# Kernel optimization log

Measured on AMD Instinct MI355X. Metric: run time of the kernel, lower is better.

## Reference

```python
import jax, jax.numpy as jnp
import numpy as np

D = 256   # hidden_dim
N = 1024  # total nodes
NP = 384  # paratope nodes
NE = 384  # epitope nodes
NC = 14   # atom channels


def setup_inputs() -> dict:
    key = jax.random.key(0)
    ks = jax.random.split(key, 24)
    s = 1.0 / np.sqrt(D)
    s3 = 1.0 / np.sqrt(3 * D)
    w = lambda k, shape, sc: (jax.random.normal(k, shape, jnp.float32) * sc)
    z = lambda: jnp.zeros((D,), jnp.float32)
    return {
        "H": w(ks[0], (N, D), 1.0),
        "X": w(ks[1], (N, NC, 3), 1.0),
        "paratope_mask": jnp.zeros((N,), bool).at[:NP].set(True),
        "epitope_mask": jnp.zeros((N,), bool).at[NP:NP + NE].set(True),
        "res_w1": w(ks[2], (1, D), 1.0), "res_b1": z(),
        "res_w2": w(ks[3], (D, D), s), "res_b2": z(),
        "atom_w1": w(ks[4], (1, D), 1.0), "atom_b1": z(),
        "atom_w2": w(ks[5], (D, D), s), "atom_b2": z(),
        "sim_weight": jnp.float32(0.5),
        "int_w1": w(ks[6], (3 * D, D), s3), "int_b1": z(),
        "int_w2": w(ks[7], (D, D), s), "int_b2": z(),
        "wl": w(ks[8], (D, D), s),
        "wr": w(ks[9], (D, D), s),
        "wg_w": w(ks[10], (D, D), s), "wg_b": z(),
        "wq_w": w(ks[11], (D, D), s), "wq_b": z(),
        "wk_w": w(ks[12], (D, D), s), "wk_b": z(),
        "wv_w": w(ks[13], (D, D), s), "wv_b": z(),
    }


def _mlp2(x, w1, b1, w2, b2):
    return jax.nn.silu(x @ w1 + b1) @ w2 + b2


def reference(H, X, paratope_mask, epitope_mask,
              res_w1, res_b1, res_w2, res_b2,
              atom_w1, atom_b1, atom_w2, atom_b2,
              sim_weight,
              int_w1, int_b1, int_w2, int_b2,
              wl, wr, wg_w, wg_b, wq_w, wq_b, wk_w, wk_b, wv_w, wv_b):
    p_idx = jnp.nonzero(paratope_mask, size=NP)[0]
    e_idx = jnp.nonzero(epitope_mask, size=NE)[0]
    Hp = H[p_idx]                      # [NP, D]
    He = H[e_idx]                      # [NE, D]
    Xp_ca = X[p_idx, 1]                # [NP, 3] (CA atom)
    Xe_ca = X[e_idx, 1]                # [NE, 3]

    dX = Xp_ca[:, None, :] - Xe_ca[None, :, :]         # [NP, NE, 3]
    S = jnp.sum(dX * dX, axis=-1, keepdims=True)       # [NP, NE, 1]
    # original computes S_residue and S_atom with identical formula
    S_res = _mlp2(S, res_w1, res_b1, res_w2, res_b2)
    S_atom = _mlp2(S, atom_w1, atom_b1, atom_w2, atom_b2)
    wmix = jax.nn.sigmoid(sim_weight)
    S_comb = wmix * S_res + (1.0 - wmix) * S_atom      # [NP, NE, D]

    Hp_e = jnp.broadcast_to(Hp[:, None, :], (NP, NE, D))
    He_e = jnp.broadcast_to(He[None, :, :], (NP, NE, D))
    Z_in = jnp.concatenate([Hp_e, He_e, S_comb], axis=-1)  # [NP, NE, 3D]
    Z = _mlp2(Z_in, int_w1, int_b1, int_w2, int_b2)        # [NP, NE, D]

    I = (Hp @ wl)[:, None, :] * (He @ wr)[None, :, :]      # outer-product interaction
    gate = jax.nn.sigmoid(Z @ wg_w + wg_b)
    f_tri = gate * I

    Q = Z @ wq_w + wq_b
    K = Z @ wk_w + wk_b
    V = Z @ wv_w + wv_b
    scores = jnp.einsum('ped,pfd->pef', Q, K) / (D ** 0.5)  # [NP, NE, NE]
    A = jax.nn.softmax(scores, axis=-1)
    f_att = jnp.einsum('pef,pfd->ped', A, V)

    H_tri = f_tri + f_att                                   # [NP, NE, D]
    return H.at[p_idx].set(H_tri.mean(axis=1))
```

## Files before the change

### kernel.cpp

```cpp
#include <hip/hip_runtime.h>

#define NPAR 384
#define NEPI 384
#define DD   256
#define NTAB 4096
#define SMAX 96.0f
#define SDELTA (SMAX / NTAB)
#define SINVD (NTAB / SMAX)

using bf16x8 = __bf16 __attribute__((ext_vector_type(8)));
using bf16x2 = __bf16 __attribute__((ext_vector_type(2)));
using f32x4  = float __attribute__((ext_vector_type(4)));

#if defined(__has_builtin)
#if __has_builtin(__builtin_amdgcn_cvt_pk_bf16_f32)
#define HAVE_PK_BF16 1
#endif
#if __has_builtin(__builtin_amdgcn_rcpf)
#define HAVE_RCPF 1
#endif
#endif

__device__ __forceinline__ float fastrcp(float x) {
#ifdef HAVE_RCPF
  return __builtin_amdgcn_rcpf(x);
#else
  return 1.0f / x;
#endif
}
__device__ __forceinline__ float sigm(float x) { return fastrcp(1.0f + __expf(-x)); }
__device__ __forceinline__ float silu(float x) { return x * fastrcp(1.0f + __expf(-x)); }
__device__ __forceinline__ unsigned short f2bf(float f) {
  unsigned u = __float_as_uint(f);
  u += 0x7fffu + ((u >> 16) & 1u);
  return (unsigned short)(u >> 16);
}
__device__ __forceinline__ float bf2f(unsigned u16) {
  return __uint_as_float(u16 << 16);
}
__device__ __forceinline__ uint2 pack4(float a, float b, float c, float d) {
  uint2 r;
#ifdef HAVE_PK_BF16
  bf16x2 lo = __builtin_amdgcn_cvt_pk_bf16_f32(a, b);
  bf16x2 hi = __builtin_amdgcn_cvt_pk_bf16_f32(c, d);
  r.x = __builtin_bit_cast(unsigned, lo);
  r.y = __builtin_bit_cast(unsigned, hi);
#else
  r.x = (unsigned)f2bf(a) | ((unsigned)f2bf(b) << 16);
  r.y = (unsigned)f2bf(c) | ((unsigned)f2bf(d) << 16);
#endif
  return r;
}

__device__ __forceinline__ void store_packed(unsigned short* __restrict__ wp,
                                             int slot, int k, int n, float v) {
  const int ks = k >> 5, lhi = (k >> 3) & 3, j = k & 7;
  const int tile = n >> 4, llo = n & 15;
  const int lane = lhi * 16 + llo;
  wp[slot * 65536 + (((ks * 16 + tile) * 64 + lane) << 3) + j] = f2bf(v);
}


__global__ void prep_kernel(
    const float* __restrict__ H, const float* __restrict__ wl,
    const float* __restrict__ wr, const float* __restrict__ int_w1,
    const float* __restrict__ res_w2, const float* __restrict__ atom_w2,
    const float* __restrict__ res_b2, const float* __restrict__ atom_b2,
    const float* __restrict__ int_b1, const float* __restrict__ simw,
    const float* __restrict__ wq_b, const float* __restrict__ wk_w,
    const float* __restrict__ wq_w, const float* __restrict__ int_w2,
    const float* __restrict__ wg_w,
    float* __restrict__ Hpl, float* __restrict__ Her,
    float* __restrict__ P1, float* __restrict__ P2,
    float* __restrict__ cvec, float* __restrict__ gv,
    unsigned short* __restrict__ wpack) {
  __shared__ float sbuf[1024];
  const int b = blockIdx.x, t = threadIdx.x;
  if (b < 256) {
    const bool isMa = b >= 128;
    const int i0 = (b & 127) * 2;
    const float wmix = 1.0f / (1.0f + __expf(-simw[0]));
    const float sc = isMa ? (1.0f - wmix) : wmix;
    const float* W2 = isMa ? atom_w2 : res_w2;
    sbuf[t] = W2[i0 * 256 + t];
    sbuf[256 + t] = W2[(i0 + 1) * 256 + t];
    __syncthreads();
    float a0 = 0.f, a1 = 0.f;
#pragma unroll 8
    for (int k = 0; k < 256; ++k) {
      const float w = int_w1[(512 + k) * 256 + t];
      a0 = fmaf(sbuf[k], w, a0);
      a1 = fmaf(sbuf[256 + k], w, a1);
    }
    const int slot = isMa ? 1 : 0;
    store_packed(wpack, slot, i0, t, a0 * sc);
    store_packed(wpack, slot, i0 + 1, t, a1 * sc);
  } else if (b == 256) {
    const float wmix = 1.0f / (1.0f + __expf(-simw[0]));
    float acc = int_b1[t];
#pragma unroll 8
    for (int k = 0; k < 256; ++k) {
      float bm = wmix * res_b2[k] + (1.0f - wmix) * atom_b2[k];
      acc += bm * int_w1[(512 + k) * 256 + t];
    }
    cvec[t] = acc;
  } else if (b < 321) {
    const int lane = t & 63, w = t >> 6;
    const int d = (b - 257) * 4 + w;
    float acc = 0.f;
#pragma unroll
    for (int i = 0; i < 4; ++i) {
      const int c = i * 64 + lane;
      acc += wk_w[d * 256 + c] * wq_b[c];
    }
    acc += __shfl_xor(acc, 1);
    acc += __shfl_xor(acc, 2);
    acc += __shfl_xor(acc, 4);
    acc += __shfl_xor(acc, 8);
    acc += __shfl_xor(acc, 16);
    acc += __shfl_xor(acc, 32);
    if (lane == 0) gv[d] = acc;
  } else if (b < 577) {
    const int r = b - 321;
    sbuf[t] = wq_w[r * 256 + t];
    __syncthreads();
    const float* wkrow = wk_w + t * 256;
    float a0 = 0.f, a1 = 0.f, a2 = 0.f, a3 = 0.f;
#pragma unroll 4
    for (int k = 0; k < 256; k += 4) {
      const f32x4 wv4 = *reinterpret_cast<const f32x4*>(&wkrow[k]);
      a0 = fmaf(sbuf[k + 0], wv4[0], a0);
      a1 = fmaf(sbuf[k + 1], wv4[1], a1);
      a2 = fmaf(sbuf[k + 2], wv4[2], a2);
      a3 = fmaf(sbuf[k + 3], wv4[3], a3);
    }
    store_packed(wpack, 4, r, t, (a0 + a1) + (a2 + a3));
  } else if (b < 961) {
    const int idx = b - 577;
    const int seg = idx / 96, r0 = (idx % 96) * 4;
    const float* A;
    const float* B;
    float* C;
    switch (seg) {
      case 0:  A = H + r0 * 256;            B = wl;              C = Hpl + r0 * 256; break;
      case 1:  A = H + (NPAR + r0) * 256;   B = wr;              C = Her + r0 * 256; break;
      case 2:  A = H + r0 * 256;            B = int_w1;          C = P1 + r0 * 256;  break;
      default: A = H + (NPAR + r0) * 256;   B = int_w1 + 65536;  C = P2 + r0 * 256;  break;
    }
#pragma unroll
    for (int j = 0; j < 4; ++j) sbuf[j * 256 + t] = A[j * 256 + t];
    __syncthreads();
    float a0 = 0.f, a1 = 0.f, a2 = 0.f, a3 = 0.f;
#pragma unroll 8
    for (int k = 0; k < 256; ++k) {
      const float bv = B[k * 256 + t];
      a0 = fmaf(sbuf[k], bv, a0);
      a1 = fmaf(sbuf[256 + k], bv, a1);
      a2 = fmaf(sbuf[512 + k], bv, a2);
      a3 = fmaf(sbuf[768 + k], bv, a3);
    }
    C[t] = a0;
    C[256 + t] = a1;
    C[512 + t] = a2;
    C[768 + t] = a3;
  } else {
    const int idx = (b - 961) * 256 + t;
    const int m = idx >> 16;
    const int r = idx & 65535;
    const int chunk = r >> 9;
    const int lane = (r >> 3) & 63;
    const int j = r & 7;
    const int k = (chunk >> 4) * 32 + (lane >> 4) * 8 + j;
    const int n = (chunk & 15) * 16 + (lane & 15);
    const float* src = (m == 0) ? int_w2 : wg_w;
    wpack[(2 + m) * 65536 + r] = f2bf(src[k * 256 + n]);
  }
}


__device__ __forceinline__ void zero_acc4(f32x4 (&acc)[4][4]) {
#pragma unroll
  for (int mt = 0; mt < 4; ++mt)
#pragma unroll
    for (int nt = 0; nt < 4; ++nt)
      acc[mt][nt] = (f32x4){0.f, 0.f, 0.f, 0.f};
}

__device__ __forceinline__ void gemm4(f32x4 (&acc)[4][4],
                                      const unsigned short* __restrict__ wp,
                                      const unsigned short* ub, int lane, int wv) {
  const int l15 = lane & 15, l4 = lane >> 4;
#pragma unroll
  for (int ks = 0; ks < 8; ++ks) {
    bf16x8 a[4];
#pragma unroll
    for (int mt = 0; mt < 4; ++mt)
      a[mt] = *reinterpret_cast<const bf16x8*>(wp + ((ks * 16 + wv * 4 + mt) * 64 + lane) * 8);
    __builtin_amdgcn_s_setprio(1);
#pragma unroll
    for (int nt = 0; nt < 4; ++nt) {
      bf16x8 b = *reinterpret_cast<const bf16x8*>(ub + (nt * 16 + l15) * 264 + ks * 32 + l4 * 8);
#pragma unroll
      for (int mt = 0; mt < 4; ++mt)
        acc[mt][nt] = __builtin_amdgcn_mfma_f32_16x16x32_bf16(a[mt], b, acc[mt][nt], 0, 0, 0);
    }
    __builtin_amdgcn_s_setprio(0);
  }
}

__device__ __forceinline__ void fill_u(unsigned short* ub, const float* Sv,
                                       const float* __restrict__ w1,
                                       const float* __restrict__ b1, int t) {
  const int dg = t & 31, rb = t >> 5;
  const f32x4 w1a = *reinterpret_cast<const f32x4*>(&w1[dg * 8]);
  const f32x4 w1b = *reinterpret_cast<const f32x4*>(&w1[dg * 8 + 4]);
  const f32x4 b1a = *reinterpret_cast<const f32x4*>(&b1[dg * 8]);
  const f32x4 b1b = *reinterpret_cast<const f32x4*>(&b1[dg * 8 + 4]);
#pragma unroll
  for (int i = 0; i < 8; ++i) {
    const int e = rb + i * 8;
    const float s = Sv[e];
    uint2 lo = pack4(silu(fmaf(s, w1a[0], b1a[0])), silu(fmaf(s, w1a[1], b1a[1])),
                     silu(fmaf(s, w1a[2], b1a[2])), silu(fmaf(s, w1a[3], b1a[3])));
    uint2 hi = pack4(silu(fmaf(s, w1b[0], b1b[0])), silu(fmaf(s, w1b[1], b1b[1])),
                     silu(fmaf(s, w1b[2], b1b[2])), silu(fmaf(s, w1b[3], b1b[3])));
    uint4 pk = {lo.x, lo.y, hi.x, hi.y};
    *reinterpret_cast<uint4*>(&ub[e * 264 + dg * 8]) = pk;
  }
}


__global__ __launch_bounds__(256, 3) void tab_kernel(
    const float* __restrict__ res_w1, const float* __restrict__ res_b1,
    const float* __restrict__ atom_w1, const float* __restrict__ atom_b1,
    const unsigned short* __restrict__ wpack, float* __restrict__ tabF) {
  __shared__ __align__(16) unsigned short ubuf[64 * 264];
  __shared__ float Sv[64];
  const int t = threadIdx.x, lane = t & 63, wv = t >> 6;
  const int l15 = lane & 15, l4 = lane >> 4;
  const int n0 = blockIdx.x * 64;
  if (t < 64) Sv[t] = (n0 + t) * SDELTA;
  __syncthreads();
  f32x4 acc[4][4];
  zero_acc4(acc);
  fill_u(ubuf, Sv, res_w1, res_b1, t);
  __syncthreads();
  gemm4(acc, wpack + 0 * 65536, ubuf, lane, wv);
  __syncthreads();
  fill_u(ubuf, Sv, atom_w1, atom_b1, t);
  __syncthreads();
  gemm4(acc, wpack + 1 * 65536, ubuf, lane, wv);
#pragma unroll
  for (int mt = 0; mt < 4; ++mt) {
    const int d = wv * 64 + mt * 16 + l4 * 4;
#pragma unroll
    for (int nt = 0; nt < 4; ++nt) {
      const int n = n0 + nt * 16 + l15;
      *reinterpret_cast<f32x4*>(&tabF[n * 256 + d]) = acc[mt][nt];
    }
  }
}


__global__ __launch_bounds__(256, 4) void pair_kernel(
    const float* __restrict__ Xg, const float* __restrict__ tabF,
    const float* __restrict__ int_b2, const float* __restrict__ wg_b,
    const unsigned short* __restrict__ wpack, const float* __restrict__ cvec,
    const float* __restrict__ P1, const float* __restrict__ P2,
    const float* __restrict__ Hpl, const float* __restrict__ Her,
    float* __restrict__ ftri, unsigned short* __restrict__ Zsw) {
  __shared__ __align__(16) unsigned short ubuf[64 * 264];
  __shared__ float Sv[64];
  __shared__ float pc[DD];
  const int t = threadIdx.x, lane = t & 63, wv = t >> 6;
  const int l15 = lane & 15, l4 = lane >> 4;
  const int wg = (blockIdx.x & 7) * 288 + (blockIdx.x >> 3);
  const int p = wg / 6, cc = wg % 6, e0 = cc * 64;
  const int d0 = wv * 64;

  if (t < 64) {
    const int e = e0 + t;
    float dx = Xg[p * 42 + 3] - Xg[(NPAR + e) * 42 + 3];
    float dy = Xg[p * 42 + 4] - Xg[(NPAR + e) * 42 + 4];
    float dz = Xg[p * 42 + 5] - Xg[(NPAR + e) * 42 + 5];
    Sv[t] = dx * dx + dy * dy + dz * dz;
  }
  pc[t] = P1[p * DD + t] + cvec[t];
  __syncthreads();

  {
    const int dg = t & 31, rb = t >> 5;
    const f32x4 pca = *reinterpret_cast<const f32x4*>(&pc[dg * 8]);
    const f32x4 pcb = *reinterpret_cast<const f32x4*>(&pc[dg * 8 + 4]);
#pragma unroll
    for (int i = 0; i < 8; ++i) {
      const int e = rb + i * 8;
      float sv = Sv[e] * SINVD;
      int idx = (int)sv;
      idx = idx > (NTAB - 2) ? (NTAB - 2) : idx;
      const float fr = sv - (float)idx;
      const f32x4 t0a = *reinterpret_cast<const f32x4*>(&tabF[idx * 256 + dg * 8]);
      const f32x4 t0b = *reinterpret_cast<const f32x4*>(&tabF[idx * 256 + dg * 8 + 4]);
      const f32x4 t1a = *reinterpret_cast<const f32x4*>(&tabF[(idx + 1) * 256 + dg * 8]);
      const f32x4 t1b = *reinterpret_cast<const f32x4*>(&tabF[(idx + 1) * 256 + dg * 8 + 4]);
      const f32x4 p2a = *reinterpret_cast<const f32x4*>(&P2[(e0 + e) * DD + dg * 8]);
      const f32x4 p2b = *reinterpret_cast<const f32x4*>(&P2[(e0 + e) * DD + dg * 8 + 4]);
      float z0 = fmaf(fr, t1a[0] - t0a[0], t0a[0]) + pca[0] + p2a[0];
      float z1 = fmaf(fr, t1a[1] - t0a[1], t0a[1]) + pca[1] + p2a[1];
      float z2 = fmaf(fr, t1a[2] - t0a[2], t0a[2]) + pca[2] + p2a[2];
      float z3 = fmaf(fr, t1a[3] - t0a[3], t0a[3]) + pca[3] + p2a[3];
      float z4 = fmaf(fr, t1b[0] - t0b[0], t0b[0]) + pcb[0] + p2b[0];
      float z5 = fmaf(fr, t1b[1] - t0b[1], t0b[1]) + pcb[1] + p2b[1];
      float z6 = fmaf(fr, t1b[2] - t0b[2], t0b[2]) + pcb[2] + p2b[2];
      float z7 = fmaf(fr, t1b[3] - t0b[3], t0b[3]) + pcb[3] + p2b[3];
      uint2 lo = pack4(silu(z0), silu(z1), silu(z2), silu(z3));
      uint2 hi = pack4(silu(z4), silu(z5), silu(z6), silu(z7));
      uint4 pk = {lo.x, lo.y, hi.x, hi.y};
      *reinterpret_cast<uint4*>(&ubuf[e * 264 + dg * 8]) = pk;
    }
  }
  __syncthreads();

  f32x4 acc[4][4];
  zero_acc4(acc);
  gemm4(acc, wpack + 2 * 65536, ubuf, lane, wv);
  __syncthreads();
#pragma unroll
  for (int mt = 0; mt < 4; ++mt) {
    const int d = d0 + mt * 16 + l4 * 4;
    const f32x4 bb = *reinterpret_cast<const f32x4*>(&int_b2[d]);
#pragma unroll
    for (int nt = 0; nt < 4; ++nt) {
      const int e = nt * 16 + l15;
      *reinterpret_cast<uint2*>(&ubuf[e * 264 + d]) =
          pack4(acc[mt][nt][0] + bb[0], acc[mt][nt][1] + bb[1],
                acc[mt][nt][2] + bb[2], acc[mt][nt][3] + bb[3]);
    }
  }
  __syncthreads();

  {
    unsigned short* Zd = Zsw + (size_t)p * 98304 + (size_t)(cc * 4 + wv) * 4096 + lane * 8;
#pragma unroll
    for (int ks = 0; ks < 8; ++ks) {
      *reinterpret_cast<uint4*>(Zd + ks * 512) =
          *reinterpret_cast<const uint4*>(&ubuf[(wv * 16 + l15) * 264 + ks * 32 + l4 * 8]);
    }
  }

  zero_acc4(acc);
  gemm4(acc, wpack + 3 * 65536, ubuf, lane, wv);
#pragma unroll
  for (int mt = 0; mt < 4; ++mt) {
    const int d = d0 + mt * 16 + l4 * 4;
    const f32x4 bb = *reinterpret_cast<const f32x4*>(&wg_b[d]);
    const f32x4 hl = *reinterpret_cast<const f32x4*>(&Hpl[p * DD + d]);
    f32x4 fs = (f32x4){0.f, 0.f, 0.f, 0.f};
#pragma unroll
    for (int nt = 0; nt < 4; ++nt) {
      const int e = e0 + nt * 16 + l15;
      const f32x4 hr = *reinterpret_cast<const f32x4*>(&Her[e * DD + d]);
#pragma unroll
      for (int r = 0; r < 4; ++r)
        fs[r] += sigm(acc[mt][nt][r] + bb[r]) * hr[r];
    }
#pragma unroll
    for (int r = 0; r < 4; ++r) {
      float v = fs[r] * hl[r];
      v += __shfl_xor(v, 1);
      v += __shfl_xor(v, 2);
      v += __shfl_xor(v, 4);
      v += __shfl_xor(v, 8);
      if (l15 == 0) atomicAdd(&ftri[p * DD + d + r], v);
    }
  }
}


__global__ __launch_bounds__(256, 4) void attn_kernel(
    const unsigned short* __restrict__ Zsw, const float* __restrict__ gv,
    const unsigned short* __restrict__ wpack, float* __restrict__ cbufg) {
  __shared__ __align__(16) unsigned short Tc[32 * 264];
  __shared__ float red[128];
  __shared__ float red2[128];
  const int t = threadIdx.x, lane = t & 63, wv = t >> 6;
  const int l15 = lane & 15, l4 = lane >> 4;
  const int xcd = blockIdx.x & 7, inner = blockIdx.x >> 3;
  const int p = (inner / 12) * 8 + xcd, c = inner % 12;
  const unsigned short* Zsp = Zsw + (size_t)p * 98304;
  const unsigned short* wqk = wpack + 4 * 65536;

  {
    f32x4 ta[4][2];
#pragma unroll
    for (int mt = 0; mt < 4; ++mt)
#pragma unroll
      for (int nt = 0; nt < 2; ++nt) ta[mt][nt] = (f32x4){0.f, 0.f, 0.f, 0.f};
    const unsigned short* Tb = Zsp + (size_t)(c * 2) * 4096 + lane * 8;
    bf16x8 bcur[2], bnxt[2];
#pragma unroll
    for (int nt = 0; nt < 2; ++nt)
      bcur[nt] = *reinterpret_cast<const bf16x8*>(Tb + nt * 4096);
#pragma unroll
    for (int ks = 0; ks < 8; ++ks) {
      if (ks < 7) {
#pragma unroll
        for (int nt = 0; nt < 2; ++nt)
          bnxt[nt] = *reinterpret_cast<const bf16x8*>(Tb + nt * 4096 + (ks + 1) * 512);
      }
      bf16x8 a[4];
#pragma unroll
      for (int mt = 0; mt < 4; ++mt)
        a[mt] = *reinterpret_cast<const bf16x8*>(wqk + ((ks * 16 + wv * 4 + mt) * 64 + lane) * 8);
      __builtin_amdgcn_s_setprio(1);
#pragma unroll
      for (int nt = 0; nt < 2; ++nt)
#pragma unroll
        for (int mt = 0; mt < 4; ++mt)
          ta[mt][nt] = __builtin_amdgcn_mfma_f32_16x16x32_bf16(a[mt], bcur[nt], ta[mt][nt], 0, 0, 0);
      __builtin_amdgcn_s_setprio(0);
      if (ks < 7) {
#pragma unroll
        for (int nt = 0; nt < 2; ++nt) bcur[nt] = bnxt[nt];
      }
    }
#pragma unroll
    for (int mt = 0; mt < 4; ++mt) {
      const int d = wv * 64 + mt * 16 + l4 * 4;
      const f32x4 gq = *reinterpret_cast<const f32x4*>(&gv[d]);
#pragma unroll
      for (int nt = 0; nt < 2; ++nt) {
        const int e = nt * 16 + l15;
        *reinterpret_cast<uint2*>(&Tc[e * 264 + d]) =
            pack4((ta[mt][nt][0] + gq[0]) * 0.0625f, (ta[mt][nt][1] + gq[1]) * 0.0625f,
                  (ta[mt][nt][2] + gq[2]) * 0.0625f, (ta[mt][nt][3] + gq[3]) * 0.0625f);
      }
    }
  }
  __syncthreads();

  f32x4 sc[2][6];
#pragma unroll
  for (int mt = 0; mt < 2; ++mt)
#pragma unroll
    for (int s = 0; s < 6; ++s) sc[mt][s] = (f32x4){0.f, 0.f, 0.f, 0.f};

  {
    const unsigned short* Sb = Zsp + (size_t)wv * 4096 + lane * 8;
    bf16x8 b0[3], b1[3];
#pragma unroll
    for (int j = 0; j < 3; ++j)
      b0[j] = *reinterpret_cast<const bf16x8*>(Sb + j * 16384);
#pragma unroll
    for (int ks = 0; ks < 8; ++ks) {
#pragma unroll
      for (int j = 0; j < 3; ++j)
        b1[j] = *reinterpret_cast<const bf16x8*>(Sb + (3 + j) * 16384 + ks * 512);
      bf16x8 a[2];
#pragma unroll
      for (int mt = 0; mt < 2; ++mt)
        a[mt] = *reinterpret_cast<const bf16x8*>(&Tc[(mt * 16 + l15) * 264 + ks * 32 + l4 * 8]);
      __builtin_amdgcn_s_setprio(1);
#pragma unroll
      for (int j = 0; j < 3; ++j)
#pragma unroll
        for (int mt = 0; mt < 2; ++mt)
          sc[mt][j] = __builtin_amdgcn_mfma_f32_16x16x32_bf16(a[mt], b0[j], sc[mt][j], 0, 0, 0);
      __builtin_amdgcn_s_setprio(0);
      if (ks < 7) {
#pragma unroll
        for (int j = 0; j < 3; ++j)
          b0[j] = *reinterpret_cast<const bf16x8*>(Sb + j * 16384 + (ks + 1) * 512);
      }
      __builtin_amdgcn_s_setprio(1);
#pragma unroll
      for (int j = 0; j < 3; ++j)
#pragma unroll
        for (int mt = 0; mt < 2; ++mt)
          sc[mt][3 + j] = __builtin_amdgcn_mfma_f32_16x16x32_bf16(a[mt], b1[j], sc[mt][3 + j], 0, 0, 0);
      __builtin_amdgcn_s_setprio(0);
    }
  }

  float rmax[2][4];
#pragma unroll
  for (int mt = 0; mt < 2; ++mt) {
#pragma unroll
    for (int r = 0; r < 4; ++r) {
      float m = -1e30f;
#pragma unroll
      for (int s = 0; s < 6; ++s) m = fmaxf(m, sc[mt][s][r]);
      m = fmaxf(m, __shfl_xor(m, 1));
      m = fmaxf(m, __shfl_xor(m, 2));
      m = fmaxf(m, __shfl_xor(m, 4));
      m = fmaxf(m, __shfl_xor(m, 8));
      rmax[mt][r] = m;
    }
  }
  if (l15 == 0) {
#pragma unroll
    for (int mt = 0; mt < 2; ++mt)
#pragma unroll
      for (int r = 0; r < 4; ++r)
        red[wv * 32 + mt * 16 + l4 * 4 + r] = rmax[mt][r];
  }
  __syncthreads();
#pragma unroll
  for (int mt = 0; mt < 2; ++mt) {
#pragma unroll
    for (int r = 0; r < 4; ++r) {
      const int row = mt * 16 + l4 * 4 + r;
      rmax[mt][r] = fmaxf(fmaxf(red[row], red[32 + row]), fmaxf(red[64 + row], red[96 + row]));
    }
  }

  float rsum[2][4];
#pragma unroll
  for (int mt = 0; mt < 2; ++mt) {
#pragma unroll
    for (int r = 0; r < 4; ++r) {
      float sSum = 0.f;
#pragma unroll
      for (int s = 0; s < 6; ++s) {
        float e = __expf(sc[mt][s][r] - rmax[mt][r]);
        sc[mt][s][r] = e;
        sSum += e;
      }
      sSum += __shfl_xor(sSum, 1);
      sSum += __shfl_xor(sSum, 2);
      sSum += __shfl_xor(sSum, 4);
      sSum += __shfl_xor(sSum, 8);
      rsum[mt][r] = sSum;
    }
  }
  if (l15 == 0) {
#pragma unroll
    for (int mt = 0; mt < 2; ++mt)
#pragma unroll
      for (int r = 0; r < 4; ++r)
        red2[wv * 32 + mt * 16 + l4 * 4 + r] = rsum[mt][r];
  }
  __syncthreads();
  float rinv[2][4];
#pragma unroll
  for (int mt = 0; mt < 2; ++mt) {
#pragma unroll
    for (int r = 0; r < 4; ++r) {
      const int row = mt * 16 + l4 * 4 + r;
      rinv[mt][r] = fastrcp(red2[row] + red2[32 + row] + red2[64 + row] + red2[96 + row]);
    }
  }

#pragma unroll
  for (int s = 0; s < 6; ++s) {
    float v = 0.f;
#pragma unroll
    for (int mt = 0; mt < 2; ++mt)
#pragma unroll
      for (int r = 0; r < 4; ++r)
        v += sc[mt][s][r] * rinv[mt][r];
    v += __shfl_xor(v, 16);
    v += __shfl_xor(v, 32);
    if (lane < 16)
      atomicAdd(&cbufg[p * NEPI + (s * 4 + wv) * 16 + lane], v);
  }
}


__global__ __launch_bounds__(256) void outa_kernel(
    const unsigned short* __restrict__ Zsw, const float* __restrict__ cbufg,
    float* __restrict__ ubufg) {
  __shared__ float cb[128];
  __shared__ float part[16][257];
  const int p = blockIdx.x / 3, th = blockIdx.x % 3, g0 = th * 8;
  const int t = threadIdx.x;
  const int lane = t & 63, wv = t >> 6;
  const int l15 = lane & 15, l4 = lane >> 4;
  if (t < 128) cb[t] = cbufg[p * NEPI + g0 * 16 + t];
  __syncthreads();
  const unsigned short* Zsp = Zsw + (size_t)p * 98304;
  float a16[16];
#pragma unroll
  for (int j = 0; j < 16; ++j) a16[j] = 0.f;
#pragma unroll
  for (int gr = 0; gr < 8; ++gr) {
    const int grp = g0 + gr;
    const float w = cb[gr * 16 + l15];
    const uint4 z0 = *reinterpret_cast<const uint4*>(Zsp + grp * 4096 + wv * 512 + lane * 8);
    const uint4 z1 = *reinterpret_cast<const uint4*>(Zsp + grp * 4096 + (wv + 4) * 512 + lane * 8);
    a16[0] = fmaf(w, bf2f(z0.x & 0xffffu), a16[0]);
    a16[1] = fmaf(w, bf2f(z0.x >> 16), a16[1]);
    a16[2] = fmaf(w, bf2f(z0.y & 0xffffu), a16[2]);
    a16[3] = fmaf(w, bf2f(z0.y >> 16), a16[3]);
    a16[4] = fmaf(w, bf2f(z0.z & 0xffffu), a16[4]);
    a16[5] = fmaf(w, bf2f(z0.z >> 16), a16[5]);
    a16[6] = fmaf(w, bf2f(z0.w & 0xffffu), a16[6]);
    a16[7] = fmaf(w, bf2f(z0.w >> 16), a16[7]);
    a16[8]  = fmaf(w, bf2f(z1.x & 0xffffu), a16[8]);
    a16[9]  = fmaf(w, bf2f(z1.x >> 16), a16[9]);
    a16[10] = fmaf(w, bf2f(z1.y & 0xffffu), a16[10]);
    a16[11] = fmaf(w, bf2f(z1.y >> 16), a16[11]);
    a16[12] = fmaf(w, bf2f(z1.z & 0xffffu), a16[12]);
    a16[13] = fmaf(w, bf2f(z1.z >> 16), a16[13]);
    a16[14] = fmaf(w, bf2f(z1.w & 0xffffu), a16[14]);
    a16[15] = fmaf(w, bf2f(z1.w >> 16), a16[15]);
  }
#pragma unroll
  for (int j = 0; j < 8; ++j) part[l15][wv * 32 + l4 * 8 + j] = a16[j];
#pragma unroll
  for (int j = 0; j < 8; ++j) part[l15][128 + wv * 32 + l4 * 8 + j] = a16[8 + j];
  __syncthreads();
  float uu = 0.f;
#pragma unroll
  for (int g = 0; g < 16; ++g) uu += part[g][t];
  atomicAdd(&ubufg[p * DD + t], uu);
}


__global__ __launch_bounds__(256) void out2_kernel(
    const float* __restrict__ ubufg, const float* __restrict__ ftri,
    const float* __restrict__ wvw, const float* __restrict__ wvb,
    float* __restrict__ out) {
  __shared__ float u[DD];
  const int p = blockIdx.x, t = threadIdx.x;
  u[t] = ubufg[p * DD + t];
  __syncthreads();
  float acc = ftri[p * DD + t] + 384.0f * wvb[t];
#pragma unroll 8
  for (int d = 0; d < DD; ++d)
    acc = fmaf(u[d], wvw[d * DD + t], acc);
  out[p * DD + t] = acc * (1.0f / 384.0f);
}


extern "C" void kernel_launch(void* const* d_in, const int* in_sizes, int n_in,
                              void* d_out, int out_size, void* d_ws, size_t ws_size,
                              hipStream_t stream) {
  (void)in_sizes; (void)n_in; (void)out_size; (void)ws_size;
  const float* H = (const float*)d_in[0];
  const float* X = (const float*)d_in[1];
  const float* res_w1 = (const float*)d_in[4];
  const float* res_b1 = (const float*)d_in[5];
  const float* res_w2 = (const float*)d_in[6];
  const float* res_b2 = (const float*)d_in[7];
  const float* atom_w1 = (const float*)d_in[8];
  const float* atom_b1 = (const float*)d_in[9];
  const float* atom_w2 = (const float*)d_in[10];
  const float* atom_b2 = (const float*)d_in[11];
  const float* simw = (const float*)d_in[12];
  const float* int_w1 = (const float*)d_in[13];
  const float* int_b1 = (const float*)d_in[14];
  const float* int_w2 = (const float*)d_in[15];
  const float* int_b2 = (const float*)d_in[16];
  const float* wl = (const float*)d_in[17];
  const float* wr = (const float*)d_in[18];
  const float* wg_w = (const float*)d_in[19];
  const float* wg_b = (const float*)d_in[20];
  const float* wq_w = (const float*)d_in[21];
  const float* wq_b = (const float*)d_in[22];
  const float* wk_w = (const float*)d_in[23];
  const float* wv_w = (const float*)d_in[25];
  const float* wv_b = (const float*)d_in[26];

  char* ws = (char*)d_ws;
  unsigned short* wpack = (unsigned short*)(ws + 0);
  float* cvec  = (float*)(ws + 655360);
  float* gv    = (float*)(ws + 656384);
  float* P1    = (float*)(ws + 657408);
  float* P2    = (float*)(ws + 1050624);
  float* Hpl   = (float*)(ws + 1443840);
  float* Her   = (float*)(ws + 1837056);
  float* ftri  = (float*)(ws + 2230272);
  float* cbufg = (float*)(ws + 2623488);
  float* ubufg = (float*)(ws + 3213312);
  unsigned short* Zsw = (unsigned short*)(ws + 3606528);
  float* tabF  = (float*)(ws + 79104000);

  hipMemsetAsync(ftri, 0, 393216 + 589824 + 393216, stream);
  prep_kernel<<<1473, 256, 0, stream>>>(H, wl, wr, int_w1, res_w2, atom_w2,
                                        res_b2, atom_b2, int_b1, simw, wq_b, wk_w,
                                        wq_w, int_w2, wg_w,
                                        Hpl, Her, P1, P2, cvec, gv, wpack);
  tab_kernel<<<NTAB / 64, 256, 0, stream>>>(res_w1, res_b1, atom_w1, atom_b1, wpack, tabF);
  pair_kernel<<<2304, 256, 0, stream>>>(X, tabF, int_b2, wg_b, wpack, cvec,
                                        P1, P2, Hpl, Her, ftri, Zsw);
  attn_kernel<<<4608, 256, 0, stream>>>(Zsw, gv, wpack, cbufg);
  outa_kernel<<<1152, 256, 0, stream>>>(Zsw, cbufg, ubufg);
  out2_kernel<<<384, 256, 0, stream>>>(ubufg, ftri, wv_w, wv_b, (float*)d_out);
  hipMemcpyAsync((float*)d_out + NPAR * DD, H + NPAR * DD,
                 (1024 - NPAR) * DD * sizeof(float), hipMemcpyDeviceToDevice, stream);
}
```

Baseline: 312.0 us.

## Swizzle pair_kernel LDS tile, drop staging arrays, raise occupancy target

The padded 264-stride LDS tile in pair_kernel becomes an unpadded 256-stride tile with an XOR swizzle on 8-element groups, applied consistently to the fill, the GEMM B-operand reads, the Z writeback and the Z export. The Sv and pc shared staging arrays and their barrier are removed; each thread now computes distances and the P1+cvec bias directly. Launch bounds rise from 4 to 5 blocks to exploit the smaller LDS footprint, which may pressure registers. The tail memcpy of untouched H rows is moved to the start of the stream.

Result: slower. 373.9 us (+19.8%).

```diff
diff --git a/kernel.cpp b/kernel.cpp
--- a/kernel.cpp
+++ b/kernel.cpp
@@ -186,6 +186,7 @@
       acc[mt][nt] = (f32x4){0.f, 0.f, 0.f, 0.f};
 }
 
+template <bool SWZ>
 __device__ __forceinline__ void gemm4(f32x4 (&acc)[4][4],
                                       const unsigned short* __restrict__ wp,
                                       const unsigned short* ub, int lane, int wv) {
@@ -199,7 +200,11 @@
     __builtin_amdgcn_s_setprio(1);
 #pragma unroll
     for (int nt = 0; nt < 4; ++nt) {
-      bf16x8 b = *reinterpret_cast<const bf16x8*>(ub + (nt * 16 + l15) * 264 + ks * 32 + l4 * 8);
+      const int row = nt * 16 + l15;
+      const unsigned short* bp =
+          SWZ ? ub + row * 256 + ((ks * 32 + l4 * 8) ^ ((row & 7) << 3))
+              : ub + row * 264 + ks * 32 + l4 * 8;
+      bf16x8 b = *reinterpret_cast<const bf16x8*>(bp);
 #pragma unroll
       for (int mt = 0; mt < 4; ++mt)
         acc[mt][nt] = __builtin_amdgcn_mfma_f32_16x16x32_bf16(a[mt], b, acc[mt][nt], 0, 0, 0);
@@ -245,11 +250,11 @@
   zero_acc4(acc);
   fill_u(ubuf, Sv, res_w1, res_b1, t);
   __syncthreads();
-  gemm4(acc, wpack + 0 * 65536, ubuf, lane, wv);
+  gemm4<false>(acc, wpack + 0 * 65536, ubuf, lane, wv);
   __syncthreads();
   fill_u(ubuf, Sv, atom_w1, atom_b1, t);
   __syncthreads();
-  gemm4(acc, wpack + 1 * 65536, ubuf, lane, wv);
+  gemm4<false>(acc, wpack + 1 * 65536, ubuf, lane, wv);
 #pragma unroll
   for (int mt = 0; mt < 4; ++mt) {
     const int d = wv * 64 + mt * 16 + l4 * 4;
@@ -262,40 +267,37 @@
 }
 
 
-__global__ __launch_bounds__(256, 4) void pair_kernel(
+__global__ __launch_bounds__(256, 5) void pair_kernel(
     const float* __restrict__ Xg, const float* __restrict__ tabF,
     const float* __restrict__ int_b2, const float* __restrict__ wg_b,
     const unsigned short* __restrict__ wpack, const float* __restrict__ cvec,
     const float* __restrict__ P1, const float* __restrict__ P2,
     const float* __restrict__ Hpl, const float* __restrict__ Her,
     float* __restrict__ ftri, unsigned short* __restrict__ Zsw) {
-  __shared__ __align__(16) unsigned short ubuf[64 * 264];
-  __shared__ float Sv[64];
-  __shared__ float pc[DD];
+  __shared__ __align__(16) unsigned short ubuf[64 * 256];
   const int t = threadIdx.x, lane = t & 63, wv = t >> 6;
   const int l15 = lane & 15, l4 = lane >> 4;
   const int wg = (blockIdx.x & 7) * 288 + (blockIdx.x >> 3);
   const int p = wg / 6, cc = wg % 6, e0 = cc * 64;
   const int d0 = wv * 64;
-
-  if (t < 64) {
-    const int e = e0 + t;
-    float dx = Xg[p * 42 + 3] - Xg[(NPAR + e) * 42 + 3];
-    float dy = Xg[p * 42 + 4] - Xg[(NPAR + e) * 42 + 4];
-    float dz = Xg[p * 42 + 5] - Xg[(NPAR + e) * 42 + 5];
-    Sv[t] = dx * dx + dy * dy + dz * dz;
-  }
-  pc[t] = P1[p * DD + t] + cvec[t];
-  __syncthreads();
+  const int dg = t & 31, rb = t >> 5;
 
   {
-    const int dg = t & 31, rb = t >> 5;
-    const f32x4 pca = *reinterpret_cast<const f32x4*>(&pc[dg * 8]);
-    const f32x4 pcb = *reinterpret_cast<const f32x4*>(&pc[dg * 8 + 4]);
+    const float qx = Xg[p * 42 + 3], qy = Xg[p * 42 + 4], qz = Xg[p * 42 + 5];
+    const f32x4 p1a = *reinterpret_cast<const f32x4*>(&P1[p * DD + dg * 8]);
+    const f32x4 p1b = *reinterpret_cast<const f32x4*>(&P1[p * DD + dg * 8 + 4]);
+    const f32x4 cva = *reinterpret_cast<const f32x4*>(&cvec[dg * 8]);
+    const f32x4 cvb = *reinterpret_cast<const f32x4*>(&cvec[dg * 8 + 4]);
+    const f32x4 pca = p1a + cva;
+    const f32x4 pcb = p1b + cvb;
 #pragma unroll
     for (int i = 0; i < 8; ++i) {
       const int e = rb + i * 8;
-      float sv = Sv[e] * SINVD;
+      const int eg = e0 + e;
+      const float dx = qx - Xg[(NPAR + eg) * 42 + 3];
+      const float dy = qy - Xg[(NPAR + eg) * 42 + 4];
+      const float dz = qz - Xg[(NPAR + eg) * 42 + 5];
+      float sv = (dx * dx + dy * dy + dz * dz) * SINVD;
       int idx = (int)sv;
       idx = idx > (NTAB - 2) ? (NTAB - 2) : idx;
       const float fr = sv - (float)idx;
@@ -303,8 +305,8 @@
       const f32x4 t0b = *reinterpret_cast<const f32x4*>(&tabF[idx * 256 + dg * 8 + 4]);
       const f32x4 t1a = *reinterpret_cast<const f32x4*>(&tabF[(idx + 1) * 256 + dg * 8]);
       const f32x4 t1b = *reinterpret_cast<const f32x4*>(&tabF[(idx + 1) * 256 + dg * 8 + 4]);
-      const f32x4 p2a = *reinterpret_cast<const f32x4*>(&P2[(e0 + e) * DD + dg * 8]);
-      const f32x4 p2b = *reinterpret_cast<const f32x4*>(&P2[(e0 + e) * DD + dg * 8 + 4]);
+      const f32x4 p2a = *reinterpret_cast<const f32x4*>(&P2[eg * DD + dg * 8]);
+      const f32x4 p2b = *reinterpret_cast<const f32x4*>(&P2[eg * DD + dg * 8 + 4]);
       float z0 = fmaf(fr, t1a[0] - t0a[0], t0a[0]) + pca[0] + p2a[0];
       float z1 = fmaf(fr, t1a[1] - t0a[1], t0a[1]) + pca[1] + p2a[1];
       float z2 = fmaf(fr, t1a[2] - t0a[2], t0a[2]) + pca[2] + p2a[2];
@@ -316,14 +318,14 @@
       uint2 lo = pack4(silu(z0), silu(z1), silu(z2), silu(z3));
       uint2 hi = pack4(silu(z4), silu(z5), silu(z6), silu(z7));
       uint4 pk = {lo.x, lo.y, hi.x, hi.y};
-      *reinterpret_cast<uint4*>(&ubuf[e * 264 + dg * 8]) = pk;
+      *reinterpret_cast<uint4*>(&ubuf[e * 256 + ((dg * 8) ^ ((e & 7) << 3))]) = pk;
     }
   }
   __syncthreads();
 
   f32x4 acc[4][4];
   zero_acc4(acc);
-  gemm4(acc, wpack + 2 * 65536, ubuf, lane, wv);
+  gemm4<true>(acc, wpack + 2 * 65536, ubuf, lane, wv);
   __syncthreads();
 #pragma unroll
   for (int mt = 0; mt < 4; ++mt) {
@@ -332,7 +334,7 @@
 #pragma unroll
     for (int nt = 0; nt < 4; ++nt) {
       const int e = nt * 16 + l15;
-      *reinterpret_cast<uint2*>(&ubuf[e * 264 + d]) =
+      *reinterpret_cast<uint2*>(&ubuf[e * 256 + (d ^ ((e & 7) << 3))]) =
           pack4(acc[mt][nt][0] + bb[0], acc[mt][nt][1] + bb[1],
                 acc[mt][nt][2] + bb[2], acc[mt][nt][3] + bb[3]);
     }
@@ -341,15 +343,16 @@
 
   {
     unsigned short* Zd = Zsw + (size_t)p * 98304 + (size_t)(cc * 4 + wv) * 4096 + lane * 8;
+    const int row = wv * 16 + l15;
 #pragma unroll
     for (int ks = 0; ks < 8; ++ks) {
-      *reinterpret_cast<uint4*>(Zd + ks * 512) =
-          *reinterpret_cast<const uint4*>(&ubuf[(wv * 16 + l15) * 264 + ks * 32 + l4 * 8]);
+      *reinterpret_cast<uint4*>(Zd + ks * 512) = *reinterpret_cast<const uint4*>(
+          &ubuf[row * 256 + ((ks * 32 + l4 * 8) ^ ((row & 7) << 3))]);
     }
   }
 
   zero_acc4(acc);
-  gemm4(acc, wpack + 3 * 65536, ubuf, lane, wv);
+  gemm4<true>(acc, wpack + 3 * 65536, ubuf, lane, wv);
 #pragma unroll
   for (int mt = 0; mt < 4; ++mt) {
     const int d = d0 + mt * 16 + l4 * 4;
@@ -676,6 +679,8 @@
   unsigned short* Zsw = (unsigned short*)(ws + 3606528);
   float* tabF  = (float*)(ws + 79104000);
 
+  hipMemcpyAsync((float*)d_out + NPAR * DD, H + NPAR * DD,
+                 (1024 - NPAR) * DD * sizeof(float), hipMemcpyDeviceToDevice, stream);
   hipMemsetAsync(ftri, 0, 393216 + 589824 + 393216, stream);
   prep_kernel<<<1473, 256, 0, stream>>>(H, wl, wr, int_w1, res_w2, atom_w2,
                                         res_b2, atom_b2, int_b1, simw, wq_b, wk_w,
@@ -687,6 +692,4 @@
   attn_kernel<<<4608, 256, 0, stream>>>(Zsw, gv, wpack, cbufg);
   outa_kernel<<<1152, 256, 0, stream>>>(Zsw, cbufg, ubufg);
   out2_kernel<<<384, 256, 0, stream>>>(ubufg, ftri, wv_w, wv_b, (float*)d_out);
-  hipMemcpyAsync((float*)d_out + NPAR * DD, H + NPAR * DD,
-                 (1024 - NPAR) * DD * sizeof(float), hipMemcpyDeviceToDevice, stream);
-}
+}
```
